# Kernel optimization log

Hardware: AMD Instinct MI355X
Metric: run time of the kernel (lower is better)

Reference implementation:

```python
import jax, jax.numpy as jnp
import numpy as np


def _consts(n_fft):
    # Static index/twiddle tables, mirroring FastIMDCT4.__init__ (numpy, host-side).
    N4 = n_fft // 4
    k = np.arange(N4)
    pre0 = 2 * k                       # even taps
    pre1 = n_fft // 2 - 1 - 2 * k      # reversed odd taps
    tw = np.exp(-2j * np.pi / n_fft * (k.astype(np.float32) + 0.125)).astype(np.complex64)
    # post-FFT de-interleave index (length n_fft, values in [0, n_fft//2))
    idx = np.empty(n_fft, np.int64)
    idx[0:n_fft // 2:2] = np.arange(0, n_fft // 2, 2)
    idx[1:n_fft // 2:2] = np.arange(n_fft // 2 - 1, 0, -2)
    idx[n_fft // 2:] = idx[:n_fft // 2][::-1]
    post = np.roll(idx, -n_fft // 4)
    # sign pattern folded into the window
    sign = np.ones(n_fft, np.float64)
    sign[1::2] *= -1.0
    sign[:n_fft // 4] *= -1.0
    sign = np.roll(sign, -n_fft // 4)
    return pre0, pre1, tw, post, sign


def setup_inputs() -> dict:
    key = jax.random.key(0)
    B, T, n_fft, hop = 32, 1024, 2048, 1024
    signal = jax.random.normal(key, (B, T, n_fft // 2), dtype=jnp.float32)
    window = jnp.ones((n_fft,), dtype=jnp.float32)  # raw window (module default: ones)
    return {"signal": signal, "window": window, "n_fft": n_fft, "hop_length": hop}


def reference(signal, window, n_fft, hop_length):
    pre0, pre1, tw, post, sign = _consts(n_fft)
    # combined window: 4 * sign * window / n_fft (module precomputes this in __init__)
    win = (4.0 * jnp.asarray(sign, jnp.float32) * window / n_fft)
    # pre-twiddle gather -> complex [B, T, n_fft//4]
    c = signal[..., pre0] + 1j * signal[..., pre1]
    twj = jnp.asarray(tw)
    c = twj * c
    c = jnp.fft.fft(c, axis=-1)
    c = twj * c
    B, T = c.shape[0], c.shape[1]
    # interleave real/imag -> [B, T, n_fft//2], then post gather -> [B, T, n_fft]
    inter = jnp.stack([jnp.real(c), jnp.imag(c)], axis=-1).reshape(B, T, n_fft // 2)
    frames = win * inter[..., post]            # [B, T, n_fft]
    # overlap-add fold (F.fold with kernel (1, n_fft), stride (1, hop))
    out_len = (T - 1) * hop_length + n_fft
    pos = (np.arange(T)[:, None] * hop_length + np.arange(n_fft)[None, :]).reshape(-1)
    out = jnp.zeros((B, out_len), frames.dtype).at[:, pos].add(frames.reshape(B, -1))
    # center=True trimming
    out = out[:, n_fft // 2: -(n_fft // 2)]
    return out[:, None, None, :]               # [B, 1, 1, (T-1)*hop], matches fold output layout
```

## Files before the change

### kernel.cpp

```cpp
#include <hip/hip_runtime.h>


#define CHUNKS 1023
#define CPB 7
#define BPB 147

__device__ __forceinline__ float2 cmul(float2 a, float2 b) {
    return make_float2(a.x * b.x - a.y * b.y, a.x * b.y + a.y * b.x);
}
__device__ __forceinline__ float2 cadd(float2 a, float2 b) {
    return make_float2(a.x + b.x, a.y + b.y);
}
__device__ __forceinline__ float2 csub(float2 a, float2 b) {
    return make_float2(a.x - b.x, a.y - b.y);
}
__device__ __forceinline__ float2 twid(float rev) {
    return make_float2(__builtin_amdgcn_cosf(rev), __builtin_amdgcn_sinf(rev));
}

__device__ __forceinline__ void postmap(int m, int& p, float& sgn) {
    bool even = ((m & 1) == 0);
    if (m < 512)       p = even ? (m + 512)  : (512 - m);
    else if (m < 1536) p = even ? (m - 511)  : (1535 - m);
    else               p = even ? (m - 1536) : (2560 - m);
    float s1 = even ? 1.0f : -1.0f;
    sgn = (m < 1536) ? s1 : -s1;
}

__device__ __forceinline__ int brev3(int r) {
    return ((r & 1) << 2) | (r & 2) | ((r >> 2) & 1);
}

__device__ __forceinline__ void fft_frame(const float* __restrict__ row, int lane,
                                          float* __restrict__ planes,
                                          const float2* __restrict__ T1,
                                          const float2* __restrict__ TS,
                                          const float2* __restrict__ TM,
                                          const float2* __restrict__ TPOST) {
    const float2* row2 = (const float2*)row;
    const int rlane = (int)(__brev((unsigned)lane) >> 26);

    float2 v[8];
    #pragma unroll
    for (int r = 0; r < 8; ++r) v[r] = row2[64 * r + rlane];

    float2 c[8];
    #pragma unroll
    for (int r = 0; r < 8; ++r) {
        float im = __shfl_xor(v[7 - r].y, 63);
        float2 tw = T1[64 * r + rlane];
        c[r] = cmul(tw, make_float2(v[r].x, im));
    }

    const float RH = 0.70710678118654752f;
    {
        float2 u0 = c[0], u1 = c[1], u2 = c[2], u3 = c[3];
        float2 l0 = c[4], l1 = c[5], l2 = c[6], l3 = c[7];
        float2 t1 = csub(u1, l1), t2 = csub(u2, l2), t3 = csub(u3, l3);
        c[0] = cadd(u0, l0); c[4] = csub(u0, l0);
        c[1] = cadd(u1, l1); c[5] = cmul(make_float2(RH, -RH), t1);
        c[2] = cadd(u2, l2); c[6] = make_float2(t2.y, -t2.x);
        c[3] = cadd(u3, l3); c[7] = cmul(make_float2(-RH, -RH), t3);
    }
    #pragma unroll
    for (int b = 0; b < 8; b += 4) {
        float2 u0 = c[b], u1 = c[b + 1], d0 = c[b + 2], d1 = c[b + 3];
        float2 t = csub(u1, d1);
        c[b] = cadd(u0, d0);
        c[b + 2] = csub(u0, d0);
        c[b + 1] = cadd(u1, d1);
        c[b + 3] = make_float2(t.y, -t.x);
    }
    #pragma unroll
    for (int b = 0; b < 8; b += 2) {
        float2 u = c[b], d = c[b + 1];
        c[b] = cadd(u, d); c[b + 1] = csub(u, d);
    }

    {
        float2 w = TM[rlane];
        float2 wc = w;
        c[4] = cmul(wc, c[4]);
        wc = cmul(wc, w); c[2] = cmul(wc, c[2]);
        wc = cmul(wc, w); c[6] = cmul(wc, c[6]);
        wc = cmul(wc, w); c[1] = cmul(wc, c[1]);
        wc = cmul(wc, w); c[5] = cmul(wc, c[5]);
        wc = cmul(wc, w); c[3] = cmul(wc, c[3]);
        wc = cmul(wc, w); c[7] = cmul(wc, c[7]);
    }

    #pragma unroll
    for (int s = 1; s <= 6; ++s) {
        const int half = 1 << (s - 1);
        const float sgn = (lane & half) ? -1.0f : 1.0f;
        float2 weff = make_float2(1.0f, 0.0f);
        if (s >= 2) weff = TS[(s - 2) * 64 + lane];
        #pragma unroll
        for (int r = 0; r < 8; ++r) {
            float2 cp = (s >= 2) ? cmul(weff, c[r]) : c[r];
            float ox = __shfl_xor(cp.x, half);
            float oy = __shfl_xor(cp.y, half);
            c[r] = make_float2(fmaf(sgn, cp.x, ox), fmaf(sgn, cp.y, oy));
        }
    }

    const float KC[8] = {1.0f,
                         0.99999529380957619f, 0.99998117528260111f,
                         0.99995764455196390f, 0.99992470183914450f,
                         0.99988234745421256f, 0.99983058179582340f,
                         0.99976940535121528f};
    const float KS[8] = {0.0f,
                         -0.0030679567629659761f, -0.0061358846491544753f,
                         -0.0092037547820598194f, -0.0122715382857199261f,
                         -0.0153392062849881011f, -0.0184067299058048209f,
                         -0.0214738704100051880f};
    float2 base = TPOST[lane];
    float2 d[8];
    #pragma unroll
    for (int j = 0; j < 8; ++j) {
        float2 tw = (j == 0) ? base : cmul(base, make_float2(KC[j], KS[j]));
        d[j] = cmul(tw, c[brev3(j)]);
    }
    float4 r0 = make_float4(d[0].x, d[1].x, d[2].x, d[3].x);
    float4 r1 = make_float4(d[4].x, d[5].x, d[6].x, d[7].x);
    float4 i0 = make_float4(d[0].y, d[1].y, d[2].y, d[3].y);
    float4 i1 = make_float4(d[4].y, d[5].y, d[6].y, d[7].y);
    *(float4*)(planes + 8 * lane)           = r0;
    *(float4*)(planes + 8 * lane + 4)       = r1;
    *(float4*)(planes + 512 + 8 * lane)     = i0;
    *(float4*)(planes + 512 + 8 * lane + 4) = i1;
}

__global__ __launch_bounds__(512) void imdct_kernel(
        const float* __restrict__ signal,
        const float* __restrict__ window,
        float* __restrict__ out) {
    __shared__ float lds[8][1024];
    __shared__ float2 T1[512];
    __shared__ float2 TS[5][64];
    __shared__ float2 TM[64];
    __shared__ float2 TPOST[64];

    const int tid = threadIdx.x;
    const int lane = tid & 63;
    const int w = tid >> 6;

    T1[tid] = twid(-((float)tid + 0.125f) * (1.0f / 2048.0f));
    if (tid < 64) {
        TM[tid]    = twid(-(float)tid * (1.0f / 512.0f));
        TPOST[tid] = twid(-((float)(8 * tid) + 0.125f) * (1.0f / 2048.0f));
    }
    if (tid < 320) {
        const int si = tid >> 6;
        const int l = tid & 63;
        const int half = 2 << si;
        float2 wv = make_float2(1.0f, 0.0f);
        if (l & half) wv = twid(-(float)(l & (half - 1)) / (float)(4 << si));
        TS[si][l] = wv;
    }
    __syncthreads();

    const int bid = blockIdx.x;
    const int b = bid / BPB;
    const int cblk = bid - b * BPB;
    const int q0 = cblk * CPB;

    const int f = q0 + w;
    if (f <= 1023) {
        fft_frame(signal + (size_t)(b * 1024 + f) * 1024, lane, &lds[w][0],
                  &T1[0], &TS[0][0], &TM[0], &TPOST[0]);
    }
    __syncthreads();

    float* orow_base = out + (size_t)b * (CHUNKS * 1024);
    const int r = 2 * tid;

    int p00, p01, p10, p11; float s00, s01, s10, s11;
    postmap(1024 + r,     p00, s00);
    postmap(1024 + r + 1, p01, s01);
    postmap(r,            p10, s10);
    postmap(r + 1,        p11, s11);
    const float2 wh = *(const float2*)(window + 1024 + r);
    const float2 wl = *(const float2*)(window + r);
    const float a00 = s00 * wh.x * (1.0f / 512.0f);
    const float a01 = s01 * wh.y * (1.0f / 512.0f);
    const float a10 = s10 * wl.x * (1.0f / 512.0f);
    const float a11 = s11 * wl.y * (1.0f / 512.0f);
    const int o00 = (p00 & 1) * 512 + (p00 >> 1);
    const int o01 = (p01 & 1) * 512 + (p01 >> 1);
    const int o10 = (p10 & 1) * 512 + (p10 >> 1);
    const int o11 = (p11 & 1) * 512 + (p11 >> 1);

    #pragma unroll
    for (int j = 0; j < CPB; ++j) {
        const int qj = q0 + j;
        if (qj > 1022) break;
        const float* f0 = &lds[j][0];
        const float* f1 = &lds[j + 1][0];
        float2 o;
        o.x = a00 * f0[o00] + a10 * f1[o10];
        o.y = a01 * f0[o01] + a11 * f1[o11];
        *(float2*)(orow_base + (size_t)qj * 1024 + r) = o;
    }
}

extern "C" void kernel_launch(void* const* d_in, const int* in_sizes, int n_in,
                              void* d_out, int out_size, void* d_ws, size_t ws_size,
                              hipStream_t stream) {
    const float* signal = (const float*)d_in[0];
    const float* window = (const float*)d_in[1];
    float* out = (float*)d_out;
    imdct_kernel<<<dim3(32 * BPB), dim3(512), 0, stream>>>(signal, window, out);
}
```

Before: 236.9 us.

## Restructure 512-point FFT as three radix-8 passes with LDS transposes

Replaces the single radix-8 pass followed by six shuffle-based radix-2 stages with three radix-8 passes. The data is exchanged through the per-wave LDS frame buffer using XOR-swizzled indices to avoid bank conflicts. Input loads become contiguous (no bit-reversed lane index), and the large twiddle tables are replaced by small tables plus constant rotations computed in registers. This aims to cut cross-lane shuffle and arithmetic cost, but adds LDS traffic and relies on implicit wave-level ordering, since only a compiler barrier separates the scratch writes from the reads.

```diff
diff --git a/kernel.cpp b/kernel.cpp
--- a/kernel.cpp
+++ b/kernel.cpp
@@ -31,27 +31,7 @@
     return ((r & 1) << 2) | (r & 2) | ((r >> 2) & 1);
 }
 
-__device__ __forceinline__ void fft_frame(const float* __restrict__ row, int lane,
-                                          float* __restrict__ planes,
-                                          const float2* __restrict__ T1,
-                                          const float2* __restrict__ TS,
-                                          const float2* __restrict__ TM,
-                                          const float2* __restrict__ TPOST) {
-    const float2* row2 = (const float2*)row;
-    const int rlane = (int)(__brev((unsigned)lane) >> 26);
-
-    float2 v[8];
-    #pragma unroll
-    for (int r = 0; r < 8; ++r) v[r] = row2[64 * r + rlane];
-
-    float2 c[8];
-    #pragma unroll
-    for (int r = 0; r < 8; ++r) {
-        float im = __shfl_xor(v[7 - r].y, 63);
-        float2 tw = T1[64 * r + rlane];
-        c[r] = cmul(tw, make_float2(v[r].x, im));
-    }
-
+__device__ __forceinline__ void radix8(float2 c[8]) {
     const float RH = 0.70710678118654752f;
     {
         float2 u0 = c[0], u1 = c[1], u2 = c[2], u3 = c[3];
@@ -76,59 +56,91 @@
         float2 u = c[b], d = c[b + 1];
         c[b] = cadd(u, d); c[b + 1] = csub(u, d);
     }
-
-    {
-        float2 w = TM[rlane];
-        float2 wc = w;
-        c[4] = cmul(wc, c[4]);
-        wc = cmul(wc, w); c[2] = cmul(wc, c[2]);
-        wc = cmul(wc, w); c[6] = cmul(wc, c[6]);
-        wc = cmul(wc, w); c[1] = cmul(wc, c[1]);
-        wc = cmul(wc, w); c[5] = cmul(wc, c[5]);
-        wc = cmul(wc, w); c[3] = cmul(wc, c[3]);
-        wc = cmul(wc, w); c[7] = cmul(wc, c[7]);
-    }
-
-    #pragma unroll
-    for (int s = 1; s <= 6; ++s) {
-        const int half = 1 << (s - 1);
-        const float sgn = (lane & half) ? -1.0f : 1.0f;
-        float2 weff = make_float2(1.0f, 0.0f);
-        if (s >= 2) weff = TS[(s - 2) * 64 + lane];
-        #pragma unroll
-        for (int r = 0; r < 8; ++r) {
-            float2 cp = (s >= 2) ? cmul(weff, c[r]) : c[r];
-            float ox = __shfl_xor(cp.x, half);
-            float oy = __shfl_xor(cp.y, half);
-            c[r] = make_float2(fmaf(sgn, cp.x, ox), fmaf(sgn, cp.y, oy));
-        }
-    }
-
-    const float KC[8] = {1.0f,
-                         0.99999529380957619f, 0.99998117528260111f,
-                         0.99995764455196390f, 0.99992470183914450f,
-                         0.99988234745421256f, 0.99983058179582340f,
-                         0.99976940535121528f};
-    const float KS[8] = {0.0f,
-                         -0.0030679567629659761f, -0.0061358846491544753f,
-                         -0.0092037547820598194f, -0.0122715382857199261f,
-                         -0.0153392062849881011f, -0.0184067299058048209f,
-                         -0.0214738704100051880f};
-    float2 base = TPOST[lane];
-    float2 d[8];
+}
+
+__device__ __forceinline__ void midchain(float2 c[8], float2 w) {
+    float2 wc = w;
+    c[4] = cmul(wc, c[4]);
+    wc = cmul(wc, w); c[2] = cmul(wc, c[2]);
+    wc = cmul(wc, w); c[6] = cmul(wc, c[6]);
+    wc = cmul(wc, w); c[1] = cmul(wc, c[1]);
+    wc = cmul(wc, w); c[5] = cmul(wc, c[5]);
+    wc = cmul(wc, w); c[3] = cmul(wc, c[3]);
+    wc = cmul(wc, w); c[7] = cmul(wc, c[7]);
+}
+
+#define K32_DECL \
+    const float K32C[8] = {1.0f, 0.98078528040323044913f, 0.92387953251128675613f, \
+                           0.83146961230254523708f, 0.70710678118654752440f,       \
+                           0.55557023301960222474f, 0.38268343236508977173f,       \
+                           0.19509032201612826785f};                               \
+    const float K32S[8] = {0.0f, -0.19509032201612826785f, -0.38268343236508977173f,\
+                           -0.55557023301960222474f, -0.70710678118654752440f,     \
+                           -0.83146961230254523708f, -0.92387953251128675613f,     \
+                           -0.98078528040323044913f};
+
+__device__ __forceinline__ void fft_frame(const float* __restrict__ row, int lane,
+                                          float* __restrict__ planes,
+                                          const float2* __restrict__ T1b,
+                                          const float2* __restrict__ TM,
+                                          const float2* __restrict__ TM2,
+                                          const float2* __restrict__ TP2) {
+    K32_DECL
+    const float2* row2 = (const float2*)row;
+    float2* scratch = (float2*)planes;
+    const int lh = lane >> 3;
+    const int ll = lane & 7;
+
+    float2 v[8];
+    #pragma unroll
+    for (int r = 0; r < 8; ++r) v[r] = row2[64 * r + lane];
+
+    float2 base = T1b[lane];
+    float2 c[8];
+    #pragma unroll
+    for (int r = 0; r < 8; ++r) {
+        float im = __shfl_xor(v[7 - r].y, 63);
+        float2 tw = (r == 0) ? base : cmul(base, make_float2(K32C[r], K32S[r]));
+        c[r] = cmul(tw, make_float2(v[r].x, im));
+    }
+
+    radix8(c);
+    midchain(c, TM[lane]);
+
+    #pragma unroll
+    for (int r = 0; r < 8; ++r) {
+        const int q = brev3(r);
+        scratch[q * 64 + ((lh ^ q)) * 8 + ll] = c[r];
+    }
+    asm volatile("" ::: "memory");
+    #pragma unroll
+    for (int r = 0; r < 8; ++r)
+        c[r] = scratch[lh * 64 + ((r ^ lh)) * 8 + ll];
+
+    radix8(c);
+    midchain(c, TM2[ll]);
+
+    #pragma unroll
+    for (int r = 0; r < 8; ++r) {
+        const int j1 = brev3(r);
+        scratch[lh * 64 + ((j1 ^ lh)) * 8 + (ll ^ j1)] = c[r];
+    }
+    asm volatile("" ::: "memory");
+    #pragma unroll
+    for (int r = 0; r < 8; ++r)
+        c[r] = scratch[lh * 64 + ((ll ^ lh)) * 8 + (r ^ ll)];
+
+    radix8(c);
+
+    float2 base2 = TP2[lane];
+    const int kbase = 8 * ll + lh;
     #pragma unroll
     for (int j = 0; j < 8; ++j) {
-        float2 tw = (j == 0) ? base : cmul(base, make_float2(KC[j], KS[j]));
-        d[j] = cmul(tw, c[brev3(j)]);
-    }
-    float4 r0 = make_float4(d[0].x, d[1].x, d[2].x, d[3].x);
-    float4 r1 = make_float4(d[4].x, d[5].x, d[6].x, d[7].x);
-    float4 i0 = make_float4(d[0].y, d[1].y, d[2].y, d[3].y);
-    float4 i1 = make_float4(d[4].y, d[5].y, d[6].y, d[7].y);
-    *(float4*)(planes + 8 * lane)           = r0;
-    *(float4*)(planes + 8 * lane + 4)       = r1;
-    *(float4*)(planes + 512 + 8 * lane)     = i0;
-    *(float4*)(planes + 512 + 8 * lane + 4) = i1;
+        float2 tw = (j == 0) ? base2 : cmul(base2, make_float2(K32C[j], K32S[j]));
+        float2 dv = cmul(tw, c[brev3(j)]);
+        planes[64 * j + kbase]       = dv.x;
+        planes[512 + 64 * j + kbase] = dv.y;
+    }
 }
 
 __global__ __launch_bounds__(512) void imdct_kernel(
@@ -136,28 +148,21 @@
         const float* __restrict__ window,
         float* __restrict__ out) {
     __shared__ float lds[8][1024];
-    __shared__ float2 T1[512];
-    __shared__ float2 TS[5][64];
+    __shared__ float2 T1b[64];
     __shared__ float2 TM[64];
-    __shared__ float2 TPOST[64];
+    __shared__ float2 TP2[64];
+    __shared__ float2 TM2[8];
 
     const int tid = threadIdx.x;
     const int lane = tid & 63;
     const int w = tid >> 6;
 
-    T1[tid] = twid(-((float)tid + 0.125f) * (1.0f / 2048.0f));
     if (tid < 64) {
-        TM[tid]    = twid(-(float)tid * (1.0f / 512.0f));
-        TPOST[tid] = twid(-((float)(8 * tid) + 0.125f) * (1.0f / 2048.0f));
-    }
-    if (tid < 320) {
-        const int si = tid >> 6;
-        const int l = tid & 63;
-        const int half = 2 << si;
-        float2 wv = make_float2(1.0f, 0.0f);
-        if (l & half) wv = twid(-(float)(l & (half - 1)) / (float)(4 << si));
-        TS[si][l] = wv;
-    }
+        T1b[tid] = twid(-((float)tid + 0.125f) * (1.0f / 2048.0f));
+        TM[tid]  = twid(-(float)tid * (1.0f / 512.0f));
+        TP2[tid] = twid(-((float)(8 * (tid & 7) + (tid >> 3)) + 0.125f) * (1.0f / 2048.0f));
+    }
+    if (tid < 8) TM2[tid] = twid(-(float)tid * (1.0f / 64.0f));
     __syncthreads();
 
     const int bid = blockIdx.x;
@@ -168,7 +173,7 @@
     const int f = q0 + w;
     if (f <= 1023) {
         fft_frame(signal + (size_t)(b * 1024 + f) * 1024, lane, &lds[w][0],
-                  &T1[0], &TS[0][0], &TM[0], &TPOST[0]);
+                  T1b, TM, TM2, TP2);
     }
     __syncthreads();
 
```

New measurement: 236.4 us. No clear change (-0.2%).
